# Performance work log

Measured on AMD Instinct MI355X. Metric: run time of the kernel, lower is better.

## Reference

```python
import jax, jax.numpy as jnp
import numpy as np

N = 100_000
E = 1_600_000
D_IN, D_H, D_L = 128, 64, 32


def _glorot(key, shape):
    fan_in, fan_out = shape[0], shape[1]
    s = jnp.sqrt(6.0 / (fan_in + fan_out)).astype(jnp.float32)
    return jax.random.uniform(key, shape, jnp.float32, -s, s)


def setup_inputs() -> dict:
    key = jax.random.key(0)
    ks = jax.random.split(key, 8)
    x = jax.random.normal(ks[0], (N, D_IN), jnp.float32)
    edge_index = jax.random.randint(ks[1], (2, E), 0, N, dtype=jnp.int64)
    return {
        "x": x,
        "edge_index": edge_index,
        "W1": _glorot(ks[2], (D_IN, D_H)),
        "b1": jnp.zeros((D_H,), jnp.float32),
        "W2": _glorot(ks[3], (D_H, D_L)),
        "b2": jnp.zeros((D_L,), jnp.float32),
        "Wd1": _glorot(ks[4], (D_L, D_H)),
        "bd1": jnp.zeros((D_H,), jnp.float32),
        "Wd2": _glorot(ks[5], (D_H, D_IN)),
        "bd2": jnp.zeros((D_IN,), jnp.float32),
    }


def gcn_conv(x, W, b, src, dst, num_nodes):
    """PyG GCNConv: add self-loops, symmetric normalization, aggregate, bias."""
    loop = jnp.arange(num_nodes, dtype=src.dtype)
    s = jnp.concatenate([src, loop])  # sources (message senders)
    d = jnp.concatenate([dst, loop])  # targets (message receivers)
    deg = jax.ops.segment_sum(jnp.ones_like(s, dtype=x.dtype), d, num_segments=num_nodes)
    dinv = jnp.where(deg > 0, jax.lax.rsqrt(deg), 0.0)
    norm = dinv[s] * dinv[d]                      # [E+N]
    h = x @ W                                     # [N, out] dense transform first
    msgs = h[s] * norm[:, None]                   # gather + scale, [E+N, out]
    out = jax.ops.segment_sum(msgs, d, num_segments=num_nodes)  # scatter-add
    return out + b


def reference(x, edge_index, W1, b1, W2, b2, Wd1, bd1, Wd2, bd2):
    src, dst = edge_index[0], edge_index[1]
    n = x.shape[0]
    z = gcn_conv(x, W1, b1, src, dst, n)
    z = jax.nn.relu(z)
    z = gcn_conv(z, W2, b2, src, dst, n)          # latent embedding
    h = jax.nn.relu(z @ Wd1 + bd1)
    reconstructed_x = h @ Wd2 + bd2
    return (reconstructed_x, z)
```

## Files before the change

kernel.cpp:

```cpp
#include <hip/hip_runtime.h>
#include <stdint.h>

#define N_NODES 100000
#define N_EDGES 1600000
#define D_INF   128
#define D_HID   64
#define D_LAT   32

typedef __attribute__((ext_vector_type(8))) short bf16x8;
typedef __attribute__((ext_vector_type(4))) float f32x4;
typedef __attribute__((ext_vector_type(8))) unsigned short u16x8;

__device__ __forceinline__ unsigned short f2bf(float v) {
  union { float f; unsigned int u; } x; x.f = v;
  unsigned int u = x.u + 0x7FFF + ((x.u >> 16) & 1);
  return (unsigned short)(u >> 16);
}
__device__ __forceinline__ float bf2f(unsigned short h) {
  union { unsigned int u; float f; } x; x.u = ((unsigned int)h) << 16;
  return x.f;
}


#define NBKT      196
#define BKT_SHIFT 9
#define BKT_CAP   10240
#define EPB       4096
#define ABLOCKS   391

__global__ void k_zerobkt(int* __restrict__ bkcnt) {
  if (threadIdx.x < NBKT) bkcnt[threadIdx.x] = 0;
}

__global__ __launch_bounds__(256) void k_binA(const int* __restrict__ esrc,
                                              const int* __restrict__ edst,
                                              int* __restrict__ bkcnt,
                                              int2* __restrict__ stage) {
  __shared__ int cnt[NBKT];
  __shared__ int sc[256];
  __shared__ int garel[NBKT];
  __shared__ int pos[NBKT];
  __shared__ __align__(16) int2 stg[EPB];
  int t = threadIdx.x;
  int e0 = blockIdx.x * EPB;

  for (int i = t; i < NBKT; i += 256) cnt[i] = 0;
  __syncthreads();

  int ds[16], ss[16];
  const int4* s4 = (const int4*)esrc;
  const int4* d4 = (const int4*)edst;
#pragma unroll
  for (int i = 0; i < 4; i++) {
    int idx4 = (e0 >> 2) + i * 256 + t;
    int4 dd = make_int4(-1, -1, -1, -1);
    int4 sv = make_int4(0, 0, 0, 0);
    if (idx4 < N_EDGES / 4) { dd = d4[idx4]; sv = s4[idx4]; }
    ds[i*4+0] = dd.x; ds[i*4+1] = dd.y; ds[i*4+2] = dd.z; ds[i*4+3] = dd.w;
    ss[i*4+0] = sv.x; ss[i*4+1] = sv.y; ss[i*4+2] = sv.z; ss[i*4+3] = sv.w;
  }
#pragma unroll
  for (int j = 0; j < 16; j++)
    if (ds[j] >= 0) atomicAdd(&cnt[ds[j] >> BKT_SHIFT], 1);
  __syncthreads();

  int c = (t < NBKT) ? cnt[t] : 0;
  sc[t] = c;
  __syncthreads();
  int incl = c;
#pragma unroll
  for (int off = 1; off < 256; off <<= 1) {
    int x = (t >= off) ? sc[t - off] : 0;
    __syncthreads();
    incl += x;
    sc[t] = incl;
    __syncthreads();
  }
  if (t < NBKT) {
    int lb = incl - c;
    int gb = 0;
    if (c > 0) gb = t * BKT_CAP + atomicAdd(&bkcnt[t], c);
    garel[t] = gb - lb;
    pos[t]   = lb;
  }
  __syncthreads();

#pragma unroll
  for (int j = 0; j < 16; j++) {
    if (ds[j] >= 0) {
      int b  = ds[j] >> BKT_SHIFT;
      int lp = atomicAdd(&pos[b], 1);
      stg[lp] = make_int2(ss[j], ds[j]);
    }
  }
  __syncthreads();

  int nval = N_EDGES - e0; if (nval > EPB) nval = EPB;
  for (int i = t; i < nval; i += 256) {
    int2 e = stg[i];
    stage[garel[e.y >> BKT_SHIFT] + i] = e;
  }
}

__global__ __launch_bounds__(512) void k_csr(const int2* __restrict__ stage,
                                             const int* __restrict__ bkcnt,
                                             int* __restrict__ beg,
                                             int* __restrict__ cnt,
                                             float* __restrict__ dinv,
                                             int* __restrict__ csr4) {
  __shared__ int hist[512];
  __shared__ int scan[512];
  int b = blockIdx.x, t = threadIdx.x;
  hist[t] = 0;
  __syncthreads();
  int n = bkcnt[b];
  int nlo = b << BKT_SHIFT;
  const int2* reg = stage + (size_t)b * BKT_CAP;
  for (int i = t; i < n; i += 512)
    atomicAdd(&hist[reg[i].y - nlo], 1);
  __syncthreads();
  int v = hist[t];
  scan[t] = v;
  __syncthreads();
  int incl = v;
#pragma unroll
  for (int off = 1; off < 512; off <<= 1) {
    int x = (t >= off) ? scan[t - off] : 0;
    __syncthreads();
    incl += x;
    scan[t] = incl;
    __syncthreads();
  }
  int loc = incl - v;
  int node = nlo + t;
  if (node < N_NODES) {
    beg[node]  = b * BKT_CAP + loc;
    cnt[node]  = v;
    dinv[node] = rsqrtf((float)(v + 1));
  }
  scan[t] = loc;
  __syncthreads();
  int* c4 = csr4 + (size_t)b * BKT_CAP;
  for (int i = t; i < n; i += 512) {
    int2 e = reg[i];
    int slot = atomicAdd(&scan[e.y - nlo], 1);
    c4[slot] = e.x;
  }
}


__global__ void k_prep_w(const float* __restrict__ W1, const float* __restrict__ W2,
                         const float* __restrict__ Wd1, const float* __restrict__ Wd2,
                         unsigned short* __restrict__ w1hi, unsigned short* __restrict__ w1lo,
                         unsigned short* __restrict__ w2hi, unsigned short* __restrict__ w2lo,
                         unsigned short* __restrict__ wd1hi, unsigned short* __restrict__ wd1lo,
                         unsigned short* __restrict__ wd2hi, unsigned short* __restrict__ wd2lo) {
  const float* src; unsigned short *hi, *lo; int K, M;
  switch (blockIdx.x) {
    case 0:  src = W1;  hi = w1hi;  lo = w1lo;  K = 128; M = 64;  break;
    case 1:  src = W2;  hi = w2hi;  lo = w2lo;  K = 64;  M = 32;  break;
    case 2:  src = Wd1; hi = wd1hi; lo = wd1lo; K = 32;  M = 64;  break;
    default: src = Wd2; hi = wd2hi; lo = wd2lo; K = 64;  M = 128; break;
  }
  int KP = K + 8;
  for (int i = threadIdx.x; i < K * M; i += 256) {
    int k = i / M, c = i % M;
    float v = src[i];
    unsigned short h = f2bf(v);
    hi[c * KP + k] = h;
    lo[c * KP + k] = f2bf(v - bf2f(h));
  }
}


template<int NODES, int K, int M>
__global__ __launch_bounds__(256) void k_mfma_gemm(const float* __restrict__ X,
                                                   const unsigned short* __restrict__ Bhi,
                                                   const unsigned short* __restrict__ Blo,
                                                   const float* __restrict__ dinv,
                                                   unsigned short* __restrict__ Y16) {
  constexpr int KP     = K + 8;
  constexpr int NSTRIP = M / 16;
  constexpr int KSTEPS = K / 32;
  constexpr int MTW    = (NODES / 16) * NSTRIP / 4;
  __shared__ __align__(16) unsigned short Ahi[NODES * KP];
  __shared__ __align__(16) unsigned short Alo[NODES * KP];

  int t = threadIdx.x;
  int node0 = blockIdx.x * NODES;

  for (int i = t; i < NODES * K / 4; i += 256) {
    int n = i / (K / 4), f4 = i % (K / 4);
    float4 v = make_float4(0.f, 0.f, 0.f, 0.f);
    if (node0 + n < N_NODES) v = ((const float4*)(X + (size_t)(node0 + n) * K))[f4];
    int base = n * KP + f4 * 4;
    float vv[4] = {v.x, v.y, v.z, v.w};
#pragma unroll
    for (int j = 0; j < 4; j++) {
      unsigned short h = f2bf(vv[j]);
      Ahi[base + j] = h;
      Alo[base + j] = f2bf(vv[j] - bf2f(h));
    }
  }
  __syncthreads();

  int w = t >> 6, lane = t & 63;
  int quad = lane >> 4, r16 = lane & 15;
  int strip = w % NSTRIP;

  bf16x8 bh[KSTEPS], bl[KSTEPS];
  const unsigned short* bp = Bhi + (strip * 16 + r16) * KP + quad * 8;
  const unsigned short* bq = Blo + (strip * 16 + r16) * KP + quad * 8;
#pragma unroll
  for (int ks = 0; ks < KSTEPS; ks++) {
    bh[ks] = *(const bf16x8*)(bp + ks * 32);
    bl[ks] = *(const bf16x8*)(bq + ks * 32);
  }

#pragma unroll
  for (int c = 0; c < MTW; c++) {
    int mt = (w / NSTRIP) * MTW + c;
    f32x4 acc = {0.f, 0.f, 0.f, 0.f};
    const unsigned short* ap = &Ahi[(mt * 16 + r16) * KP + quad * 8];
    const unsigned short* aq = &Alo[(mt * 16 + r16) * KP + quad * 8];
#pragma unroll
    for (int ks = 0; ks < KSTEPS; ks++) {
      bf16x8 ah = *(const bf16x8*)(ap + ks * 32);
      bf16x8 al = *(const bf16x8*)(aq + ks * 32);
      acc = __builtin_amdgcn_mfma_f32_16x16x32_bf16(ah, bh[ks], acc, 0, 0, 0);
      acc = __builtin_amdgcn_mfma_f32_16x16x32_bf16(ah, bl[ks], acc, 0, 0, 0);
      acc = __builtin_amdgcn_mfma_f32_16x16x32_bf16(al, bh[ks], acc, 0, 0, 0);
    }
    int gn  = node0 + mt * 16 + quad * 4;
    int col = strip * 16 + r16;
#pragma unroll
    for (int r = 0; r < 4; r++) {
      if (gn + r < N_NODES)
        Y16[(size_t)(gn + r) * M + col] = f2bf(acc[r] * dinv[gn + r]);
    }
  }
}


template<int FEAT, bool RELU>
__global__ __launch_bounds__(256) void k_aggregate(const unsigned short* __restrict__ H16,
                            const int* __restrict__ beg,
                            const int* __restrict__ cnt,
                            const int* __restrict__ csr4,
                            const float* __restrict__ dinv, const float* __restrict__ bias,
                            float* __restrict__ OUT) {
  constexpr int LPE    = FEAT / 8;
  constexpr int GROUPS = 64 / LPE;

  int node = blockIdx.x * 4 + (threadIdx.x >> 6);
  int lane = threadIdx.x & 63;
  if (node >= N_NODES) return;
  int bg = beg[node], end = bg + cnt[node];
  int g  = lane / LPE;
  int f8 = lane % LPE;

  float a0=0.f,a1=0.f,a2=0.f,a3=0.f,a4=0.f,a5=0.f,a6=0.f,a7=0.f;

  for (int p = bg; p < end; p += 2 * GROUPS) {
    int q0 = p + g, q1 = p + GROUPS + g;
    int s0 = (q0 < end) ? csr4[q0] : node;
    int s1 = (q1 < end) ? csr4[q1] : node;
    float m0 = (q0 < end) ? 1.f : 0.f;
    float m1 = (q1 < end) ? 1.f : 0.f;
    u16x8 h0 = *(const u16x8*)(H16 + (size_t)s0 * FEAT + f8 * 8);
    u16x8 h1 = *(const u16x8*)(H16 + (size_t)s1 * FEAT + f8 * 8);
    a0 += bf2f(h0[0]) * m0; a1 += bf2f(h0[1]) * m0;
    a2 += bf2f(h0[2]) * m0; a3 += bf2f(h0[3]) * m0;
    a4 += bf2f(h0[4]) * m0; a5 += bf2f(h0[5]) * m0;
    a6 += bf2f(h0[6]) * m0; a7 += bf2f(h0[7]) * m0;
    a0 += bf2f(h1[0]) * m1; a1 += bf2f(h1[1]) * m1;
    a2 += bf2f(h1[2]) * m1; a3 += bf2f(h1[3]) * m1;
    a4 += bf2f(h1[4]) * m1; a5 += bf2f(h1[5]) * m1;
    a6 += bf2f(h1[6]) * m1; a7 += bf2f(h1[7]) * m1;
  }

#pragma unroll
  for (int off = LPE; off < 64; off <<= 1) {
    a0 += __shfl_xor(a0, off, 64);
    a1 += __shfl_xor(a1, off, 64);
    a2 += __shfl_xor(a2, off, 64);
    a3 += __shfl_xor(a3, off, 64);
    a4 += __shfl_xor(a4, off, 64);
    a5 += __shfl_xor(a5, off, 64);
    a6 += __shfl_xor(a6, off, 64);
    a7 += __shfl_xor(a7, off, 64);
  }

  if (g == 0) {
    float di = dinv[node];
    u16x8 hs = *(const u16x8*)(H16 + (size_t)node * FEAT + f8 * 8);
    float4 bv0 = *(const float4*)(bias + f8 * 8);
    float4 bv1 = *(const float4*)(bias + f8 * 8 + 4);
    a0 = (a0 + bf2f(hs[0])) * di + bv0.x;
    a1 = (a1 + bf2f(hs[1])) * di + bv0.y;
    a2 = (a2 + bf2f(hs[2])) * di + bv0.z;
    a3 = (a3 + bf2f(hs[3])) * di + bv0.w;
    a4 = (a4 + bf2f(hs[4])) * di + bv1.x;
    a5 = (a5 + bf2f(hs[5])) * di + bv1.y;
    a6 = (a6 + bf2f(hs[6])) * di + bv1.z;
    a7 = (a7 + bf2f(hs[7])) * di + bv1.w;
    if (RELU) {
      a0 = fmaxf(a0, 0.f); a1 = fmaxf(a1, 0.f);
      a2 = fmaxf(a2, 0.f); a3 = fmaxf(a3, 0.f);
      a4 = fmaxf(a4, 0.f); a5 = fmaxf(a5, 0.f);
      a6 = fmaxf(a6, 0.f); a7 = fmaxf(a7, 0.f);
    }
    float4 o0; o0.x = a0; o0.y = a1; o0.z = a2; o0.w = a3;
    float4 o1; o1.x = a4; o1.y = a5; o1.z = a6; o1.w = a7;
    *(float4*)(OUT + (size_t)node * FEAT + f8 * 8)     = o0;
    *(float4*)(OUT + (size_t)node * FEAT + f8 * 8 + 4) = o1;
  }
}


__global__ __launch_bounds__(256) void k_decoder_mfma(
    const float* __restrict__ Z,
    const unsigned short* __restrict__ B1hi, const unsigned short* __restrict__ B1lo,
    const float* __restrict__ bd1,
    const unsigned short* __restrict__ B2hi, const unsigned short* __restrict__ B2lo,
    const float* __restrict__ bd2, float* __restrict__ RECON) {
  constexpr int KP1 = 40;
  constexpr int KP2 = 72;
  __shared__ __align__(16) unsigned short Azhi[64 * KP1];
  __shared__ __align__(16) unsigned short Azlo[64 * KP1];
  __shared__ __align__(16) unsigned short H3hi[64 * KP2];
  __shared__ __align__(16) unsigned short H3lo[64 * KP2];
  int t = threadIdx.x;
  int node0 = blockIdx.x * 64;

  for (int i = t; i < 512; i += 256) {
    int n = i >> 3, f4 = i & 7;
    float4 v = make_float4(0.f, 0.f, 0.f, 0.f);
    if (node0 + n < N_NODES) v = ((const float4*)(Z + (size_t)(node0 + n) * 32))[f4];
    int base = n * KP1 + f4 * 4;
    float vv[4] = {v.x, v.y, v.z, v.w};
#pragma unroll
    for (int j = 0; j < 4; j++) {
      unsigned short h = f2bf(vv[j]);
      Azhi[base + j] = h;
      Azlo[base + j] = f2bf(vv[j] - bf2f(h));
    }
  }
  __syncthreads();

  int w = t >> 6, lane = t & 63;
  int quad = lane >> 4, r16 = lane & 15;

  {
    int col = w * 16 + r16;
    float bias1 = bd1[col];
    bf16x8 bh = *(const bf16x8*)(B1hi + col * KP1 + quad * 8);
    bf16x8 bl = *(const bf16x8*)(B1lo + col * KP1 + quad * 8);
#pragma unroll
    for (int m = 0; m < 4; m++) {
      bf16x8 ah = *(const bf16x8*)(Azhi + (m * 16 + r16) * KP1 + quad * 8);
      bf16x8 al = *(const bf16x8*)(Azlo + (m * 16 + r16) * KP1 + quad * 8);
      f32x4 acc = {0.f, 0.f, 0.f, 0.f};
      acc = __builtin_amdgcn_mfma_f32_16x16x32_bf16(ah, bh, acc, 0, 0, 0);
      acc = __builtin_amdgcn_mfma_f32_16x16x32_bf16(ah, bl, acc, 0, 0, 0);
      acc = __builtin_amdgcn_mfma_f32_16x16x32_bf16(al, bh, acc, 0, 0, 0);
#pragma unroll
      for (int r = 0; r < 4; r++) {
        int row = m * 16 + quad * 4 + r;
        float hv = fmaxf(acc[r] + bias1, 0.f);
        unsigned short h = f2bf(hv);
        H3hi[row * KP2 + col] = h;
        H3lo[row * KP2 + col] = f2bf(hv - bf2f(h));
      }
    }
  }
  __syncthreads();

#pragma unroll
  for (int sp = 0; sp < 2; sp++) {
    int strip = w + sp * 4;
    int col = strip * 16 + r16;
    float bias2 = bd2[col];
    const unsigned short* b2h = B2hi + col * KP2 + quad * 8;
    const unsigned short* b2l = B2lo + col * KP2 + quad * 8;
    bf16x8 bh0 = *(const bf16x8*)(b2h);
    bf16x8 bh1 = *(const bf16x8*)(b2h + 32);
    bf16x8 bl0 = *(const bf16x8*)(b2l);
    bf16x8 bl1 = *(const bf16x8*)(b2l + 32);
#pragma unroll
    for (int m = 0; m < 4; m++) {
      const unsigned short* ahp = H3hi + (m * 16 + r16) * KP2 + quad * 8;
      const unsigned short* alp = H3lo + (m * 16 + r16) * KP2 + quad * 8;
      bf16x8 ah0 = *(const bf16x8*)(ahp);
      bf16x8 ah1 = *(const bf16x8*)(ahp + 32);
      bf16x8 al0 = *(const bf16x8*)(alp);
      bf16x8 al1 = *(const bf16x8*)(alp + 32);
      f32x4 acc = {0.f, 0.f, 0.f, 0.f};
      acc = __builtin_amdgcn_mfma_f32_16x16x32_bf16(ah0, bh0, acc, 0, 0, 0);
      acc = __builtin_amdgcn_mfma_f32_16x16x32_bf16(ah1, bh1, acc, 0, 0, 0);
      acc = __builtin_amdgcn_mfma_f32_16x16x32_bf16(ah0, bl0, acc, 0, 0, 0);
      acc = __builtin_amdgcn_mfma_f32_16x16x32_bf16(ah1, bl1, acc, 0, 0, 0);
      acc = __builtin_amdgcn_mfma_f32_16x16x32_bf16(al0, bh0, acc, 0, 0, 0);
      acc = __builtin_amdgcn_mfma_f32_16x16x32_bf16(al1, bh1, acc, 0, 0, 0);
#pragma unroll
      for (int r = 0; r < 4; r++) {
        int n = node0 + m * 16 + quad * 4 + r;
        if (n < N_NODES) RECON[(size_t)n * 128 + col] = acc[r] + bias2;
      }
    }
  }
}


extern "C" void kernel_launch(void* const* d_in, const int* in_sizes, int n_in,
                              void* d_out, int out_size, void* d_ws, size_t ws_size,
                              hipStream_t stream) {
  const float* x    = (const float*)d_in[0];
  const int*   eidx = (const int*)d_in[1];
  const int*   esrc = eidx;
  const int*   edst = eidx + N_EDGES;
  const float* W1  = (const float*)d_in[2];
  const float* b1  = (const float*)d_in[3];
  const float* W2  = (const float*)d_in[4];
  const float* b2  = (const float*)d_in[5];
  const float* Wd1 = (const float*)d_in[6];
  const float* bd1 = (const float*)d_in[7];
  const float* Wd2 = (const float*)d_in[8];
  const float* bd2 = (const float*)d_in[9];

  float* recon = (float*)d_out;
  float* z     = (float*)d_out + (size_t)N_NODES * D_INF;
  int2*           stage = (int2*)recon;
  unsigned short* h1_16 = (unsigned short*)recon;
  float*          z1    = (float*)((char*)recon + 12800000);
  unsigned short* h2_16 = (unsigned short*)((char*)recon + 38400000);

  char* ws = (char*)d_ws;
  int*   beg    = (int*)(ws + 0);
  int*   cntn   = (int*)(ws + 409600);
  float* dinv   = (float*)(ws + 819200);
  int*   bkcnt  = (int*)(ws + 1228800);
  int*   csr4   = (int*)(ws + 1229824);
  unsigned short* w1hi  = (unsigned short*)(ws + 9257984);
  unsigned short* w1lo  = (unsigned short*)(ws + 9275392);
  unsigned short* w2hi  = (unsigned short*)(ws + 9292800);
  unsigned short* w2lo  = (unsigned short*)(ws + 9297408);
  unsigned short* wd1hi = (unsigned short*)(ws + 9302016);
  unsigned short* wd1lo = (unsigned short*)(ws + 9307136);
  unsigned short* wd2hi = (unsigned short*)(ws + 9312256);
  unsigned short* wd2lo = (unsigned short*)(ws + 9330688);

  k_zerobkt<<<1, 256, 0, stream>>>(bkcnt);
  k_binA<<<ABLOCKS, 256, 0, stream>>>(esrc, edst, bkcnt, stage);
  k_csr<<<NBKT, 512, 0, stream>>>(stage, bkcnt, beg, cntn, dinv, csr4);
  k_prep_w<<<4, 256, 0, stream>>>(W1, W2, Wd1, Wd2, w1hi, w1lo, w2hi, w2lo,
                                  wd1hi, wd1lo, wd2hi, wd2lo);

  k_mfma_gemm<64, 128, 64><<<(N_NODES + 63) / 64, 256, 0, stream>>>(x, w1hi, w1lo, dinv, h1_16);
  k_aggregate<64, true><<<(N_NODES + 3) / 4, 256, 0, stream>>>(h1_16, beg, cntn, csr4, dinv, b1, z1);
  k_mfma_gemm<64, 64, 32><<<(N_NODES + 63) / 64, 256, 0, stream>>>(z1, w2hi, w2lo, dinv, h2_16);
  k_aggregate<32, false><<<(N_NODES + 3) / 4, 256, 0, stream>>>(h2_16, beg, cntn, csr4, dinv, b2, z);
  k_decoder_mfma<<<(N_NODES + 63) / 64, 256, 0, stream>>>(z, wd1hi, wd1lo, bd1,
                                                          wd2hi, wd2lo, bd2, recon);
}
```

Baseline: 290.0 us.

## Pack staged edges, merge zeroing into weight prep, widen CSR and aggregate batching

Staged edges are now packed into one int (source shifted left by 9 bits, local destination in the low bits) instead of an int2, which halves staging traffic between binning and CSR build. The bucket-counter zeroing is folded into the weight-prep kernel as an extra block, removing one launch. Binning blocks are halved in size and doubled in count, and the CSR kernel moves to 1024 threads. The aggregate loop now issues four neighbour gathers per iteration instead of two for more memory-level parallelism, at the cost of extra registers. Packing relies on source indices fitting in 23 bits, which holds for N=100000.

```diff
diff --git a/kernel.cpp b/kernel.cpp
--- a/kernel.cpp
+++ b/kernel.cpp
@@ -25,17 +25,13 @@
 #define NBKT      196
 #define BKT_SHIFT 9
 #define BKT_CAP   10240
-#define EPB       4096
-#define ABLOCKS   391
-
-__global__ void k_zerobkt(int* __restrict__ bkcnt) {
-  if (threadIdx.x < NBKT) bkcnt[threadIdx.x] = 0;
-}
+#define EPB       2048
+#define ABLOCKS   782
 
 __global__ __launch_bounds__(256) void k_binA(const int* __restrict__ esrc,
                                               const int* __restrict__ edst,
                                               int* __restrict__ bkcnt,
-                                              int2* __restrict__ stage) {
+                                              int* __restrict__ stage) {
   __shared__ int cnt[NBKT];
   __shared__ int sc[256];
   __shared__ int garel[NBKT];
@@ -47,11 +43,11 @@
   for (int i = t; i < NBKT; i += 256) cnt[i] = 0;
   __syncthreads();
 
-  int ds[16], ss[16];
+  int ds[8], ss[8];
   const int4* s4 = (const int4*)esrc;
   const int4* d4 = (const int4*)edst;
 #pragma unroll
-  for (int i = 0; i < 4; i++) {
+  for (int i = 0; i < 2; i++) {
     int idx4 = (e0 >> 2) + i * 256 + t;
     int4 dd = make_int4(-1, -1, -1, -1);
     int4 sv = make_int4(0, 0, 0, 0);
@@ -60,7 +56,7 @@
     ss[i*4+0] = sv.x; ss[i*4+1] = sv.y; ss[i*4+2] = sv.z; ss[i*4+3] = sv.w;
   }
 #pragma unroll
-  for (int j = 0; j < 16; j++)
+  for (int j = 0; j < 8; j++)
     if (ds[j] >= 0) atomicAdd(&cnt[ds[j] >> BKT_SHIFT], 1);
   __syncthreads();
 
@@ -86,7 +82,7 @@
   __syncthreads();
 
 #pragma unroll
-  for (int j = 0; j < 16; j++) {
+  for (int j = 0; j < 8; j++) {
     if (ds[j] >= 0) {
       int b  = ds[j] >> BKT_SHIFT;
       int lp = atomicAdd(&pos[b], 1);
@@ -98,53 +94,54 @@
   int nval = N_EDGES - e0; if (nval > EPB) nval = EPB;
   for (int i = t; i < nval; i += 256) {
     int2 e = stg[i];
-    stage[garel[e.y >> BKT_SHIFT] + i] = e;
-  }
-}
-
-__global__ __launch_bounds__(512) void k_csr(const int2* __restrict__ stage,
-                                             const int* __restrict__ bkcnt,
-                                             int* __restrict__ beg,
-                                             int* __restrict__ cnt,
-                                             float* __restrict__ dinv,
-                                             int* __restrict__ csr4) {
+    stage[garel[e.y >> BKT_SHIFT] + i] = (e.x << BKT_SHIFT) | (e.y & 511);
+  }
+}
+
+__global__ __launch_bounds__(1024) void k_csr(const int* __restrict__ stage,
+                                              const int* __restrict__ bkcnt,
+                                              int* __restrict__ beg,
+                                              int* __restrict__ cnt,
+                                              float* __restrict__ dinv,
+                                              int* __restrict__ csr4) {
   __shared__ int hist[512];
   __shared__ int scan[512];
   int b = blockIdx.x, t = threadIdx.x;
-  hist[t] = 0;
+  if (t < 512) hist[t] = 0;
   __syncthreads();
   int n = bkcnt[b];
   int nlo = b << BKT_SHIFT;
-  const int2* reg = stage + (size_t)b * BKT_CAP;
-  for (int i = t; i < n; i += 512)
-    atomicAdd(&hist[reg[i].y - nlo], 1);
-  __syncthreads();
-  int v = hist[t];
-  scan[t] = v;
+  const int* reg = stage + (size_t)b * BKT_CAP;
+  for (int i = t; i < n; i += 1024)
+    atomicAdd(&hist[reg[i] & 511], 1);
+  __syncthreads();
+  int v = (t < 512) ? hist[t] : 0;
+  if (t < 512) scan[t] = v;
   __syncthreads();
   int incl = v;
 #pragma unroll
   for (int off = 1; off < 512; off <<= 1) {
-    int x = (t >= off) ? scan[t - off] : 0;
+    int x = (t >= off && t < 512) ? scan[t - off] : 0;
     __syncthreads();
-    incl += x;
-    scan[t] = incl;
+    if (t < 512) { incl += x; scan[t] = incl; }
     __syncthreads();
   }
-  int loc = incl - v;
-  int node = nlo + t;
-  if (node < N_NODES) {
-    beg[node]  = b * BKT_CAP + loc;
-    cnt[node]  = v;
-    dinv[node] = rsqrtf((float)(v + 1));
-  }
-  scan[t] = loc;
+  if (t < 512) {
+    int loc = incl - v;
+    int node = nlo + t;
+    if (node < N_NODES) {
+      beg[node]  = b * BKT_CAP + loc;
+      cnt[node]  = v;
+      dinv[node] = rsqrtf((float)(v + 1));
+    }
+    scan[t] = loc;
+  }
   __syncthreads();
   int* c4 = csr4 + (size_t)b * BKT_CAP;
-  for (int i = t; i < n; i += 512) {
-    int2 e = reg[i];
-    int slot = atomicAdd(&scan[e.y - nlo], 1);
-    c4[slot] = e.x;
+  for (int i = t; i < n; i += 1024) {
+    int e = reg[i];
+    int slot = atomicAdd(&scan[e & 511], 1);
+    c4[slot] = e >> BKT_SHIFT;
   }
 }
 
@@ -154,7 +151,12 @@
                          unsigned short* __restrict__ w1hi, unsigned short* __restrict__ w1lo,
                          unsigned short* __restrict__ w2hi, unsigned short* __restrict__ w2lo,
                          unsigned short* __restrict__ wd1hi, unsigned short* __restrict__ wd1lo,
-                         unsigned short* __restrict__ wd2hi, unsigned short* __restrict__ wd2lo) {
+                         unsigned short* __restrict__ wd2hi, unsigned short* __restrict__ wd2lo,
+                         int* __restrict__ bkcnt) {
+  if (blockIdx.x == 4) {
+    if (threadIdx.x < NBKT) bkcnt[threadIdx.x] = 0;
+    return;
+  }
   const float* src; unsigned short *hi, *lo; int K, M;
   switch (blockIdx.x) {
     case 0:  src = W1;  hi = w1hi;  lo = w1lo;  K = 128; M = 64;  break;
@@ -261,22 +263,28 @@
 
   float a0=0.f,a1=0.f,a2=0.f,a3=0.f,a4=0.f,a5=0.f,a6=0.f,a7=0.f;
 
-  for (int p = bg; p < end; p += 2 * GROUPS) {
-    int q0 = p + g, q1 = p + GROUPS + g;
-    int s0 = (q0 < end) ? csr4[q0] : node;
-    int s1 = (q1 < end) ? csr4[q1] : node;
-    float m0 = (q0 < end) ? 1.f : 0.f;
-    float m1 = (q1 < end) ? 1.f : 0.f;
-    u16x8 h0 = *(const u16x8*)(H16 + (size_t)s0 * FEAT + f8 * 8);
-    u16x8 h1 = *(const u16x8*)(H16 + (size_t)s1 * FEAT + f8 * 8);
-    a0 += bf2f(h0[0]) * m0; a1 += bf2f(h0[1]) * m0;
-    a2 += bf2f(h0[2]) * m0; a3 += bf2f(h0[3]) * m0;
-    a4 += bf2f(h0[4]) * m0; a5 += bf2f(h0[5]) * m0;
-    a6 += bf2f(h0[6]) * m0; a7 += bf2f(h0[7]) * m0;
-    a0 += bf2f(h1[0]) * m1; a1 += bf2f(h1[1]) * m1;
-    a2 += bf2f(h1[2]) * m1; a3 += bf2f(h1[3]) * m1;
-    a4 += bf2f(h1[4]) * m1; a5 += bf2f(h1[5]) * m1;
-    a6 += bf2f(h1[6]) * m1; a7 += bf2f(h1[7]) * m1;
+  for (int p = bg; p < end; p += 4 * GROUPS) {
+    int   sarr[4];
+    float marr[4];
+    u16x8 harr[4];
+#pragma unroll
+    for (int b4 = 0; b4 < 4; b4++) {
+      int q = p + b4 * GROUPS + g;
+      sarr[b4] = (q < end) ? csr4[q] : node;
+      marr[b4] = (q < end) ? 1.f : 0.f;
+    }
+#pragma unroll
+    for (int b4 = 0; b4 < 4; b4++)
+      harr[b4] = *(const u16x8*)(H16 + (size_t)sarr[b4] * FEAT + f8 * 8);
+#pragma unroll
+    for (int b4 = 0; b4 < 4; b4++) {
+      float m = marr[b4];
+      u16x8 h = harr[b4];
+      a0 += bf2f(h[0]) * m; a1 += bf2f(h[1]) * m;
+      a2 += bf2f(h[2]) * m; a3 += bf2f(h[3]) * m;
+      a4 += bf2f(h[4]) * m; a5 += bf2f(h[5]) * m;
+      a6 += bf2f(h[6]) * m; a7 += bf2f(h[7]) * m;
+    }
   }
 
 #pragma unroll
@@ -430,7 +438,7 @@
 
   float* recon = (float*)d_out;
   float* z     = (float*)d_out + (size_t)N_NODES * D_INF;
-  int2*           stage = (int2*)recon;
+  int*            stage = (int*)recon;
   unsigned short* h1_16 = (unsigned short*)recon;
   float*          z1    = (float*)((char*)recon + 12800000);
   unsigned short* h2_16 = (unsigned short*)((char*)recon + 38400000);
@@ -450,11 +458,10 @@
   unsigned short* wd2hi = (unsigned short*)(ws + 9312256);
   unsigned short* wd2lo = (unsigned short*)(ws + 9330688);
 
-  k_zerobkt<<<1, 256, 0, stream>>>(bkcnt);
+  k_prep_w<<<5, 256, 0, stream>>>(W1, W2, Wd1, Wd2, w1hi, w1lo, w2hi, w2lo,
+                                  wd1hi, wd1lo, wd2hi, wd2lo, bkcnt);
   k_binA<<<ABLOCKS, 256, 0, stream>>>(esrc, edst, bkcnt, stage);
-  k_csr<<<NBKT, 512, 0, stream>>>(stage, bkcnt, beg, cntn, dinv, csr4);
-  k_prep_w<<<4, 256, 0, stream>>>(W1, W2, Wd1, Wd2, w1hi, w1lo, w2hi, w2lo,
-                                  wd1hi, wd1lo, wd2hi, wd2lo);
+  k_csr<<<NBKT, 1024, 0, stream>>>(stage, bkcnt, beg, cntn, dinv, csr4);
 
   k_mfma_gemm<64, 128, 64><<<(N_NODES + 63) / 64, 256, 0, stream>>>(x, w1hi, w1lo, dinv, h1_16);
   k_aggregate<64, true><<<(N_NODES + 3) / 4, 256, 0, stream>>>(h1_16, beg, cntn, csr4, dinv, b1, z1);
```

Result: no change. 291.1 us (+0.4%).
